# Performance work log

Measured on AMD Instinct MI355X. Metric: run time of the kernel, lower is better.

Reference implementation:

```python
import jax, jax.numpy as jnp
import numpy as np
from jax import lax

B, E, DIN = 16, 1024, 128   # batch, num_edges, link_state_dim
P, D = 2048, 128            # num_paths, path_state_dim


def _topology():
    # deterministic ragged paths: lengths in [4,16], at least one of max length 16
    lengths = 4 + (np.arange(P) % 13)
    idx = np.repeat(np.arange(P), lengths).astype(np.int32)          # path id per entry
    seqs = np.concatenate([np.arange(l) for l in lengths]).astype(np.int32)  # position in path
    paths = np.random.RandomState(0).randint(0, E, size=idx.shape[0]).astype(np.int32)
    return paths, idx, seqs


def setup_inputs() -> dict:
    key = jax.random.key(0)
    ks = jax.random.split(key, 8)
    paths, idx, seqs = _topology()
    s_in = 1.0 / np.sqrt(DIN)
    s_h = 1.0 / np.sqrt(D)
    return dict(
        inputs=jax.random.normal(ks[0], (B, E, DIN), jnp.float32),
        W_in=jax.random.normal(ks[1], (DIN, 3 * D), jnp.float32) * s_in,
        W_rec=jax.random.normal(ks[2], (D, 3 * D), jnp.float32) * s_h,
        b_in=jnp.zeros((3 * D,), jnp.float32),
        b_rec=jnp.zeros((3 * D,), jnp.float32),
        wq=jax.random.normal(ks[3], (D, D), jnp.float32) * s_h,
        wk=jax.random.normal(ks[4], (D, D), jnp.float32) * s_h,
        wv=jax.random.normal(ks[5], (D, D), jnp.float32) * s_h,
        paths=paths, idx=idx, seqs=seqs,
    )


def _forward(inputs, W_in, W_rec, b_in, b_rec, wq, wk, wv, paths, idx, seqs, max_len):
    Bc = inputs.shape[0]
    # --- ragged gather -> dense zero-padded tensor [B, P, max_len, DIN] (tf.gather + scatter_nd) ---
    h_tild = inputs[:, paths]                                  # [B, n_entries, DIN]
    link = jnp.zeros((Bc, P, max_len, DIN), inputs.dtype)
    link = link.at[:, idx, seqs].set(h_tild)
    x = link.reshape(Bc * P, max_len, DIN)                     # [BP, L, DIN]
    # --- GRU over time (keras GRUCell default: reset_after=True, tanh/sigmoid) ---
    xg = jnp.einsum('nld,de->lne', x, W_in) + b_in             # [L, BP, 3D]
    h0 = jnp.zeros((Bc * P, D), inputs.dtype)

    def step(h, xg_t):
        hg = h @ W_rec + b_rec                                 # [BP, 3D]
        xz, xr, xh = jnp.split(xg_t, 3, axis=-1)
        hz, hr, hh = jnp.split(hg, 3, axis=-1)
        z = jax.nn.sigmoid(xz + hz)
        r = jax.nn.sigmoid(xr + hr)
        hc = jnp.tanh(xh + r * hh)
        hn = z * h + (1.0 - z) * hc
        return hn, hn

    last, hs = lax.scan(step, h0, xg)                          # last:[BP,D], hs:[L,BP,D]
    hs = jnp.transpose(hs, (1, 0, 2))                          # [BP, L, D]
    # --- single-query QKV attention (raw scores, no softmax, as in source) ---
    key_ = hs @ wk                                             # [BP, L, D]
    val = hs @ wv                                              # [BP, L, D]
    q = last @ wq                                              # [BP, D]
    att = jnp.einsum('nld,nd->nl', key_, q)                    # [BP, L]
    ctx = jnp.einsum('nl,nld->nd', att, val)                   # [BP, D]
    return ctx.reshape(Bc, P, D)


def reference(inputs, W_in, W_rec, b_in, b_rec, wq, wk, wv, paths, idx, seqs):
    max_len = int(np.max(np.asarray(seqs))) + 1                # static (16)
    return _forward(inputs, W_in, W_rec, b_in, b_rec, wq, wk, wv, paths, idx, seqs, max_len)
```

## Files before the change

kernel.cpp:

```cpp
#include <hip/hip_runtime.h>
#include <hip/hip_bf16.h>
#include <cstddef>

#define P_ 2048
#define B_ 16
#define E_ 1024
#define D_ 128
#define L_ 16
#define TD_ 384

#define NEG_L2E (-1.44269504088896340736f)
#define TWO_L2E (2.88539008177792681472f)

typedef _Float16 f16x2 __attribute__((ext_vector_type(2)));
typedef _Float16 f16x8 __attribute__((ext_vector_type(8)));
typedef float    f32x4 __attribute__((ext_vector_type(4)));

__device__ __forceinline__ unsigned short f2h(float x) {
    _Float16 h = (_Float16)x;
    return __builtin_bit_cast(unsigned short, h);
}
__device__ __forceinline__ unsigned pk2(float a, float b) {
    return __builtin_bit_cast(unsigned, __builtin_amdgcn_cvt_pkrtz(a, b));
}
__device__ __forceinline__ float lo16(unsigned u) {
    return (float)__builtin_bit_cast(f16x2, u)[0];
}
__device__ __forceinline__ float hi16(unsigned u) {
    return (float)__builtin_bit_cast(f16x2, u)[1];
}
__device__ __forceinline__ float ex2(float x) {
#if __has_builtin(__builtin_amdgcn_exp2f)
    return __builtin_amdgcn_exp2f(x);
#else
    return exp2f(x);
#endif
}
__device__ __forceinline__ float dot2w(unsigned hu, unsigned qu, float c) {
#if __has_builtin(__builtin_amdgcn_fdot2)
    typedef __fp16 h2v __attribute__((ext_vector_type(2)));
    return __builtin_amdgcn_fdot2(__builtin_bit_cast(h2v, hu),
                                  __builtin_bit_cast(h2v, qu), c, false);
#else
    f16x2 h = __builtin_bit_cast(f16x2, hu), q = __builtin_bit_cast(f16x2, qu);
    return c + (float)h[0] * (float)q[0] + (float)h[1] * (float)q[1];
#endif
}

__device__ __forceinline__ void binv4(const float* __restrict__ d, float* __restrict__ o) {
    float f1 = d[0] * d[1];
    float f2 = f1 * d[2];
    float f3 = f2 * d[3];
    float r  = __builtin_amdgcn_rcpf(f3);
    o[3] = r * f2;
    float t  = r * d[3];
    o[2] = t * f1;
    float u  = t * d[2];
    o[1] = u * d[0];
    o[0] = u * d[1];
}

__device__ __forceinline__ void wf16(const float* __restrict__ src,
                                     unsigned short* __restrict__ dst, int g, int N,
                                     float sc) {
    int lane = g & 63, kt = (g >> 6) & 3, tile = g >> 8;
    int k0 = kt * 32 + (lane >> 4) * 8;
    int c = tile * 16 + (lane & 15);
#pragma unroll
    for (int j = 0; j < 8; ++j)
        dst[(size_t)g * 8 + j] = f2h(src[(size_t)(k0 + j) * N + c] * sc);
}

__device__ __forceinline__ void* hp(void* base, int t, int s, int boff) {
    return (char*)base + ((t * 16 + s) << 8) + (boff ^ ((s & 7) << 4));
}
__device__ __forceinline__ const void* hpc(const void* base, int t, int s, int boff) {
    return (const char*)base + ((t * 16 + s) << 8) + (boff ^ ((s & 7) << 4));
}

__global__ __launch_bounds__(256) void k_prep(const float* __restrict__ W_rec,
                                              const float* __restrict__ W_in,
                                              const float* __restrict__ wq,
                                              const float* __restrict__ wk,
                                              const float* __restrict__ wv,
                                              const int* __restrict__ paths,
                                              int* __restrict__ pt,
                                              unsigned short* __restrict__ WfR,
                                              unsigned short* __restrict__ WfI,
                                              unsigned short* __restrict__ wvf,
                                              float* __restrict__ M) {
    __shared__ float wk_lds[128 * 129];
    __shared__ float wq_row2[2][128];
    int blk = blockIdx.x, tid = threadIdx.x;
    if (blk < 128) {
        int gid = blk * 256 + tid;
        int p = gid >> 4, s = gid & 15;
        int c = p / 13, r = p - c * 13;
        int len = 4 + r;
        int off = 4 * p + 78 * c + (r * (r - 1)) / 2;
        pt[gid] = (s < len) ? paths[off + s] : E_;
        return;
    } else if (blk < 152) {
        int gg = (blk - 128) * 256 + tid;
        wf16(W_rec, WfR, gg, TD_, ((gg >> 8) < 16) ? NEG_L2E : TWO_L2E);
        return;
    } else if (blk < 176) {
        int gg = (blk - 152) * 256 + tid;
        wf16(W_in, WfI, gg, TD_, ((gg >> 8) < 16) ? NEG_L2E : TWO_L2E);
        return;
    } else if (blk < 184) {
        wf16(wv, wvf, (blk - 176) * 256 + tid, 128, 1.f);
        return;
    }
    int j0 = (blk - 184) * 2;
    int d = tid & 127, half = tid >> 7;
    for (int r = half * 64; r < half * 64 + 64; ++r)
        wk_lds[r * 129 + d] = wk[r * 128 + d];
    wq_row2[half][d] = wq[(j0 + half) * 128 + d];
    __syncthreads();
    float acc = 0.f;
    for (int k = 0; k < 128; ++k) acc += wq_row2[half][k] * wk_lds[d * 129 + k];
    M[(j0 + half) * 128 + d] = acc;
}

__global__ __launch_bounds__(256) void k_G(const float* __restrict__ inputs,
                                           const unsigned short* __restrict__ WfI,
                                           const float* __restrict__ b_in,
                                           const float* __restrict__ b_rec,
                                           unsigned short* __restrict__ G2,
                                           const float* __restrict__ M,
                                           unsigned short* __restrict__ Mf) {
    if (blockIdx.x >= 1024) {
        int tb = blockIdx.x - 1024;
        if (tb < 8) {
            wf16(M, Mf, tb * 256 + threadIdx.x, 128, 1.f);
        } else {
            for (int i = threadIdx.x; i < 2048; i += 256) {
                int bx = i >> 7, cc = i & 127;
                size_t base = ((size_t)(bx * (E_ + 1) + E_) * 128 + cc) * 4;
                G2[base]     = f2h((b_in[cc] + b_rec[cc]) * NEG_L2E);
                G2[base + 1] = f2h((b_in[128 + cc] + b_rec[128 + cc]) * NEG_L2E);
                G2[base + 2] = f2h(b_in[256 + cc] * TWO_L2E);
                G2[base + 3] = 0;
            }
        }
        return;
    }
    __shared__ __align__(16) unsigned short a_lds[16][136];
    __shared__ __align__(16) unsigned short g_lds[16][128][4];
    int tid = threadIdx.x, w = tid >> 6, L = tid & 63;
    int l15 = L & 15, q = L >> 4;
    int row0 = blockIdx.x * 16;
    int badd = row0 >> 10;
    {
        int r = tid >> 4, c = (tid & 15) * 8;
        const float4* p = (const float4*)(inputs + (size_t)(row0 + r) * 128 + c);
        float4 v0 = p[0], v1 = p[1];
        uint4 st;
        st.x = pk2(v0.x, v0.y); st.y = pk2(v0.z, v0.w);
        st.z = pk2(v1.x, v1.y); st.w = pk2(v1.z, v1.w);
        *(uint4*)&a_lds[r][c] = st;
    }
    __syncthreads();
    f16x8 af[4];
#pragma unroll
    for (int kt = 0; kt < 4; ++kt)
        af[kt] = *(const f16x8*)&a_lds[l15][kt * 32 + q * 8];
#pragma unroll
    for (int ct = 0; ct < 6; ++ct) {
        int tl = 6 * w + ct;
        f32x4 acc = (f32x4){0.f, 0.f, 0.f, 0.f};
#pragma unroll
        for (int kt = 0; kt < 4; ++kt)
            acc = __builtin_amdgcn_mfma_f32_16x16x32_f16(
                af[kt], *(const f16x8*)(WfI + (size_t)((tl * 4 + kt) * 64 + L) * 8), acc, 0, 0, 0);
        int g  = tl >> 3;
        int dd = (tl & 7) * 16 + l15;
        float sg  = (g < 2) ? NEG_L2E : TWO_L2E;
        float bia = (b_in[tl * 16 + l15] + (g < 2 ? b_rec[tl * 16 + l15] : 0.f)) * sg;
#pragma unroll
        for (int j = 0; j < 4; ++j) {
            int r = q * 4 + j;
            g_lds[r][dd][g] = f2h(acc[j] + bia);
        }
    }
    __syncthreads();
    {
        const uint4* src = (const uint4*)g_lds;
        uint4* dst = (uint4*)(G2 + (size_t)(row0 + badd) * 512);
#pragma unroll
        for (int i = 0; i < 4; ++i) dst[tid + 256 * i] = src[tid + 256 * i];
    }
}

__global__ __launch_bounds__(512, 4) void k_rec(const unsigned short* __restrict__ WfR,
                                                const float* __restrict__ b_rec,
                                                const unsigned short* __restrict__ G2,
                                                const int* __restrict__ pt,
                                                const unsigned short* __restrict__ Mf,
                                                const unsigned short* __restrict__ wvf,
                                                float* __restrict__ out) {
    __shared__ __align__(16) unsigned short hsl[16][16][128];
    __shared__ __align__(16) unsigned short qkb[16][136];
    __shared__ __align__(16) unsigned short svb[16][136];
    __shared__ float attp[2][16][16];
    __shared__ int ofs_lds[16][16];

    int tid = threadIdx.x, w = tid >> 6, L = tid & 63;
    int l15 = L & 15, q = L >> 4;
    int c0 = 16 * w + 4 * q;
    int n0 = blockIdx.x * 16;
    int b  = n0 >> 11;
    int p0 = n0 & (P_ - 1);
    int bb = b * (E_ + 1);

    f16x8 afw[3][4];
#pragma unroll
    for (int g = 0; g < 3; ++g)
#pragma unroll
        for (int kt = 0; kt < 4; ++kt)
            afw[g][kt] = *(const f16x8*)(WfR + (size_t)(((g * 8 + w) * 4 + kt) * 64 + L) * 8);

    if (tid < 256)
        ofs_lds[tid >> 4][tid & 15] = (bb + pt[p0 * L_ + tid]) << 10;

    f32x4 rh4;
#pragma unroll
    for (int j = 0; j < 4; ++j) rh4[j] = b_rec[256 + c0 + j] * TWO_L2E;
    float h_reg[4] = {0.f, 0.f, 0.f, 0.f};
    __syncthreads();

    int ofs[16];
    {
        const uint4* op = (const uint4*)&ofs_lds[l15][0];
        uint4 o0 = op[0], o1 = op[1], o2 = op[2], o3 = op[3];
        ofs[0]  = o0.x; ofs[1]  = o0.y; ofs[2]  = o0.z; ofs[3]  = o0.w;
        ofs[4]  = o1.x; ofs[5]  = o1.y; ofs[6]  = o1.z; ofs[7]  = o1.w;
        ofs[8]  = o2.x; ofs[9]  = o2.y; ofs[10] = o2.z; ofs[11] = o2.w;
        ofs[12] = o3.x; ofs[13] = o3.y; ofs[14] = o3.z; ofs[15] = o3.w;
    }

    const char* g2c = (const char*)G2 + (size_t)c0 * 8;
    uint4 cur0 = *(const uint4*)(g2c + ofs[0]);
    uint4 cur1 = *(const uint4*)(g2c + ofs[0] + 16);

#pragma unroll
    for (int t = 0; t < L_; ++t) {
        uint4 nx0 = cur0, nx1 = cur1;
        if (t < 15) {
            const char* gp = g2c + ofs[t + 1];
            nx0 = *(const uint4*)(gp);
            nx1 = *(const uint4*)(gp + 16);
        }

        float xh[4];
        f32x4 acc[3];
        acc[0][0] = lo16(cur0.x); acc[0][1] = lo16(cur0.z);
        acc[0][2] = lo16(cur1.x); acc[0][3] = lo16(cur1.z);
        acc[1][0] = hi16(cur0.x); acc[1][1] = hi16(cur0.z);
        acc[1][2] = hi16(cur1.x); acc[1][3] = hi16(cur1.z);
        xh[0] = lo16(cur0.y); xh[1] = lo16(cur0.w);
        xh[2] = lo16(cur1.y); xh[3] = lo16(cur1.w);
        acc[2] = rh4;

        if (t > 0) {
            f16x8 hf[4];
#pragma unroll
            for (int kt = 0; kt < 4; ++kt)
                hf[kt] = *(const f16x8*)hpc(hsl, t - 1, l15, kt * 64 + q * 16);
#pragma unroll
            for (int g = 0; g < 3; ++g)
#pragma unroll
                for (int kt = 0; kt < 4; ++kt)
                    acc[g] = __builtin_amdgcn_mfma_f32_16x16x32_f16(afw[g][kt], hf[kt], acc[g], 0, 0, 0);
        }

        float dz[4], dr[4];
#pragma unroll
        for (int j = 0; j < 4; ++j) {
            dz[j] = 1.f + ex2(acc[0][j]);
            dr[j] = 1.f + ex2(acc[1][j]);
        }
        float z4[4], r4[4];
        binv4(dz, z4);
        binv4(dr, r4);
        float dh[4];
#pragma unroll
        for (int j = 0; j < 4; ++j)
            dh[j] = 1.f + ex2(fminf(xh[j] + r4[j] * acc[2][j], 30.f));
        float y4[4];
        binv4(dh, y4);
        float hn[4];
#pragma unroll
        for (int j = 0; j < 4; ++j) {
            float hc = 1.f - 2.f * y4[j];
            hn[j] = hc + z4[j] * (h_reg[j] - hc);
            h_reg[j] = hn[j];
        }
        uint2 st;
        st.x = pk2(hn[0], hn[1]); st.y = pk2(hn[2], hn[3]);
        *(uint2*)hp(hsl, t, l15, c0 * 2) = st;
        cur0 = nx0; cur1 = nx1;

        __builtin_amdgcn_wave_barrier();
        __builtin_amdgcn_s_waitcnt(0xC07F);
        __builtin_amdgcn_s_barrier();
        __builtin_amdgcn_wave_barrier();
    }

    {
        f16x8 hf[4];
#pragma unroll
        for (int kt = 0; kt < 4; ++kt)
            hf[kt] = *(const f16x8*)hpc(hsl, 15, l15, kt * 64 + q * 16);
        f32x4 a = (f32x4){0.f, 0.f, 0.f, 0.f};
#pragma unroll
        for (int kt = 0; kt < 4; ++kt)
            a = __builtin_amdgcn_mfma_f32_16x16x32_f16(
                *(const f16x8*)(Mf + (size_t)((w * 4 + kt) * 64 + L) * 8), hf[kt], a, 0, 0, 0);
        uint2 st;
        st.x = pk2(a[0], a[1]); st.y = pk2(a[2], a[3]);
        *(uint2*)&qkb[l15][c0] = st;
    }
    __syncthreads();

    {
        int s = tid & 15, l = (tid >> 4) & 15, half = tid >> 8;
        const uint4* qr = (const uint4*)&qkb[s][half * 64];
        float a = 0.f;
#pragma unroll
        for (int k8 = 0; k8 < 8; ++k8) {
            uint4 hh = *(const uint4*)hpc(hsl, l, s, half * 128 + k8 * 16);
            uint4 qq = qr[k8];
            a = dot2w(hh.x, qq.x, a); a = dot2w(hh.y, qq.y, a);
            a = dot2w(hh.z, qq.z, a); a = dot2w(hh.w, qq.w, a);
        }
        attp[half][s][l] = a;
    }
    __syncthreads();

    {
        int s = tid >> 5, d0 = (tid & 31) * 4;
        float v[4] = {0.f, 0.f, 0.f, 0.f};
#pragma unroll
        for (int l = 0; l < 16; ++l) {
            float a = attp[0][s][l] + attp[1][s][l];
            uint2 hu = *(const uint2*)hpc(hsl, l, s, d0 * 2);
            v[0] += a * lo16(hu.x); v[1] += a * hi16(hu.x);
            v[2] += a * lo16(hu.y); v[3] += a * hi16(hu.y);
        }
        uint2 st;
        st.x = pk2(v[0], v[1]); st.y = pk2(v[2], v[3]);
        *(uint2*)&svb[s][d0] = st;
    }
    __syncthreads();

    {
        f16x8 sf[4];
#pragma unroll
        for (int kt = 0; kt < 4; ++kt)
            sf[kt] = *(const f16x8*)&svb[l15][kt * 32 + q * 8];
        f32x4 a = (f32x4){0.f, 0.f, 0.f, 0.f};
#pragma unroll
        for (int kt = 0; kt < 4; ++kt)
            a = __builtin_amdgcn_mfma_f32_16x16x32_f16(
                *(const f16x8*)(wvf + (size_t)((w * 4 + kt) * 64 + L) * 8), sf[kt], a, 0, 0, 0);
        *(f32x4*)&out[(size_t)(n0 + l15) * D_ + c0] = a;
    }
}

extern "C" void kernel_launch(void* const* d_in, const int* in_sizes, int n_in,
                              void* d_out, int out_size, void* d_ws, size_t ws_size,
                              hipStream_t stream) {
    const float* inputs = (const float*)d_in[0];
    const float* W_in   = (const float*)d_in[1];
    const float* W_rec  = (const float*)d_in[2];
    const float* b_in   = (const float*)d_in[3];
    const float* b_rec  = (const float*)d_in[4];
    const float* wq     = (const float*)d_in[5];
    const float* wk     = (const float*)d_in[6];
    const float* wvp    = (const float*)d_in[7];
    const int* paths    = (const int*)d_in[8];

    const size_t off_pt  = 0;
    const size_t off_WfR = off_pt  + (size_t)P_ * L_ * 4;
    const size_t off_WfI = off_WfR + (size_t)24 * 256 * 16;
    const size_t off_Mf  = off_WfI + (size_t)24 * 256 * 16;
    const size_t off_wvf = off_Mf  + (size_t)8 * 256 * 16;
    const size_t off_M   = off_wvf + (size_t)8 * 256 * 16;
    const size_t off_G2  = off_M   + (size_t)128 * 128 * 4;
    char* ws = (char*)d_ws;
    int* pt             = (int*)(ws + off_pt);
    unsigned short* WfR = (unsigned short*)(ws + off_WfR);
    unsigned short* WfI = (unsigned short*)(ws + off_WfI);
    unsigned short* Mf  = (unsigned short*)(ws + off_Mf);
    unsigned short* wvf = (unsigned short*)(ws + off_wvf);
    float* M            = (float*)(ws + off_M);
    unsigned short* G2  = (unsigned short*)(ws + off_G2);
    float* out = (float*)d_out;

    k_prep<<<dim3(248), dim3(256), 0, stream>>>(W_rec, W_in, wq, wk, wvp, paths,
                                                pt, WfR, WfI, wvf, M);
    k_G<<<dim3(1024 + 8 + 1), dim3(256), 0, stream>>>(inputs, WfI, b_in, b_rec,
                                                      G2, M, Mf);
    k_rec<<<dim3(B_ * P_ / 16), dim3(512), 0, stream>>>(WfR, b_rec, G2, pt,
                                                        Mf, wvf, out);
}
```

Measured before the change: 173.6 us.

## Rebalance prep work across kernels, cut k_rec registers, drop batched reciprocals

Moves the path-table, W_rec and wv conversions out of k_prep into extra blocks of k_G, and has k_prep write M straight into the fp16 MFMA layout, so the separate fp32 M buffer and its conversion pass go away. In k_rec, the 16 per-lane gather offsets are now read from LDS each step instead of being held in registers. The batched reciprocal trick (binv4) is replaced by one rcp per gate element. The launch-bounds hint for k_rec drops from 4 to 2 waves per SIMD, which lets the compiler use more registers, possibly at the cost of occupancy.

```diff
diff --git a/kernel.cpp b/kernel.cpp
--- a/kernel.cpp
+++ b/kernel.cpp
@@ -47,19 +47,6 @@
 #endif
 }
 
-__device__ __forceinline__ void binv4(const float* __restrict__ d, float* __restrict__ o) {
-    float f1 = d[0] * d[1];
-    float f2 = f1 * d[2];
-    float f3 = f2 * d[3];
-    float r  = __builtin_amdgcn_rcpf(f3);
-    o[3] = r * f2;
-    float t  = r * d[3];
-    o[2] = t * f1;
-    float u  = t * d[2];
-    o[1] = u * d[0];
-    o[0] = u * d[1];
-}
-
 __device__ __forceinline__ void wf16(const float* __restrict__ src,
                                      unsigned short* __restrict__ dst, int g, int N,
                                      float sc) {
@@ -78,41 +65,20 @@
     return (const char*)base + ((t * 16 + s) << 8) + (boff ^ ((s & 7) << 4));
 }
 
-__global__ __launch_bounds__(256) void k_prep(const float* __restrict__ W_rec,
-                                              const float* __restrict__ W_in,
+__global__ __launch_bounds__(256) void k_prep(const float* __restrict__ W_in,
                                               const float* __restrict__ wq,
                                               const float* __restrict__ wk,
-                                              const float* __restrict__ wv,
-                                              const int* __restrict__ paths,
-                                              int* __restrict__ pt,
-                                              unsigned short* __restrict__ WfR,
                                               unsigned short* __restrict__ WfI,
-                                              unsigned short* __restrict__ wvf,
-                                              float* __restrict__ M) {
+                                              unsigned short* __restrict__ Mf) {
     __shared__ float wk_lds[128 * 129];
     __shared__ float wq_row2[2][128];
     int blk = blockIdx.x, tid = threadIdx.x;
-    if (blk < 128) {
-        int gid = blk * 256 + tid;
-        int p = gid >> 4, s = gid & 15;
-        int c = p / 13, r = p - c * 13;
-        int len = 4 + r;
-        int off = 4 * p + 78 * c + (r * (r - 1)) / 2;
-        pt[gid] = (s < len) ? paths[off + s] : E_;
-        return;
-    } else if (blk < 152) {
-        int gg = (blk - 128) * 256 + tid;
-        wf16(W_rec, WfR, gg, TD_, ((gg >> 8) < 16) ? NEG_L2E : TWO_L2E);
-        return;
-    } else if (blk < 176) {
-        int gg = (blk - 152) * 256 + tid;
+    if (blk < 24) {
+        int gg = blk * 256 + tid;
         wf16(W_in, WfI, gg, TD_, ((gg >> 8) < 16) ? NEG_L2E : TWO_L2E);
         return;
-    } else if (blk < 184) {
-        wf16(wv, wvf, (blk - 176) * 256 + tid, 128, 1.f);
-        return;
-    }
-    int j0 = (blk - 184) * 2;
+    }
+    int j0 = (blk - 24) * 2;
     int d = tid & 127, half = tid >> 7;
     for (int r = half * 64; r < half * 64 + 64; ++r)
         wk_lds[r * 129 + d] = wk[r * 128 + d];
@@ -120,7 +86,12 @@
     __syncthreads();
     float acc = 0.f;
     for (int k = 0; k < 128; ++k) acc += wq_row2[half][k] * wk_lds[d * 129 + k];
-    M[(j0 + half) * 128 + d] = acc;
+    {
+        int r = j0 + half;
+        int tile = d >> 4, kt = r >> 5;
+        int ln = ((r >> 3) & 3) * 16 + (d & 15), jj = r & 7;
+        Mf[((size_t)(tile * 4 + kt) * 64 + ln) * 8 + jj] = f2h(acc);
+    }
 }
 
 __global__ __launch_bounds__(256) void k_G(const float* __restrict__ inputs,
@@ -128,14 +99,28 @@
                                            const float* __restrict__ b_in,
                                            const float* __restrict__ b_rec,
                                            unsigned short* __restrict__ G2,
-                                           const float* __restrict__ M,
-                                           unsigned short* __restrict__ Mf) {
+                                           const float* __restrict__ W_rec,
+                                           const float* __restrict__ wv,
+                                           const int* __restrict__ paths,
+                                           int* __restrict__ pt,
+                                           unsigned short* __restrict__ WfR,
+                                           unsigned short* __restrict__ wvf) {
     if (blockIdx.x >= 1024) {
-        int tb = blockIdx.x - 1024;
-        if (tb < 8) {
-            wf16(M, Mf, tb * 256 + threadIdx.x, 128, 1.f);
+        int tb = blockIdx.x - 1024, tid = threadIdx.x;
+        if (tb < 128) {
+            int gid = tb * 256 + tid;
+            int p = gid >> 4, s = gid & 15;
+            int c = p / 13, r = p - c * 13;
+            int len = 4 + r;
+            int off = 4 * p + 78 * c + (r * (r - 1)) / 2;
+            pt[gid] = (s < len) ? paths[off + s] : E_;
+        } else if (tb < 152) {
+            int gg = (tb - 128) * 256 + tid;
+            wf16(W_rec, WfR, gg, TD_, ((gg >> 8) < 16) ? NEG_L2E : TWO_L2E);
+        } else if (tb < 160) {
+            wf16(wv, wvf, (tb - 152) * 256 + tid, 128, 1.f);
         } else {
-            for (int i = threadIdx.x; i < 2048; i += 256) {
+            for (int i = tid; i < 2048; i += 256) {
                 int bx = i >> 7, cc = i & 127;
                 size_t base = ((size_t)(bx * (E_ + 1) + E_) * 128 + cc) * 4;
                 G2[base]     = f2h((b_in[cc] + b_rec[cc]) * NEG_L2E);
@@ -193,7 +178,7 @@
     }
 }
 
-__global__ __launch_bounds__(512, 4) void k_rec(const unsigned short* __restrict__ WfR,
+__global__ __launch_bounds__(512, 2) void k_rec(const unsigned short* __restrict__ WfR,
                                                 const float* __restrict__ b_rec,
                                                 const unsigned short* __restrict__ G2,
                                                 const int* __restrict__ pt,
@@ -230,25 +215,18 @@
     float h_reg[4] = {0.f, 0.f, 0.f, 0.f};
     __syncthreads();
 
-    int ofs[16];
-    {
-        const uint4* op = (const uint4*)&ofs_lds[l15][0];
-        uint4 o0 = op[0], o1 = op[1], o2 = op[2], o3 = op[3];
-        ofs[0]  = o0.x; ofs[1]  = o0.y; ofs[2]  = o0.z; ofs[3]  = o0.w;
-        ofs[4]  = o1.x; ofs[5]  = o1.y; ofs[6]  = o1.z; ofs[7]  = o1.w;
-        ofs[8]  = o2.x; ofs[9]  = o2.y; ofs[10] = o2.z; ofs[11] = o2.w;
-        ofs[12] = o3.x; ofs[13] = o3.y; ofs[14] = o3.z; ofs[15] = o3.w;
-    }
-
     const char* g2c = (const char*)G2 + (size_t)c0 * 8;
-    uint4 cur0 = *(const uint4*)(g2c + ofs[0]);
-    uint4 cur1 = *(const uint4*)(g2c + ofs[0] + 16);
+    int ocur = ofs_lds[l15][0];
+    uint4 cur0 = *(const uint4*)(g2c + ocur);
+    uint4 cur1 = *(const uint4*)(g2c + ocur + 16);
 
 #pragma unroll
     for (int t = 0; t < L_; ++t) {
         uint4 nx0 = cur0, nx1 = cur1;
+        int onext = ocur;
         if (t < 15) {
-            const char* gp = g2c + ofs[t + 1];
+            onext = ofs_lds[l15][t + 1];
+            const char* gp = g2c + onext;
             nx0 = *(const uint4*)(gp);
             nx1 = *(const uint4*)(gp + 16);
         }
@@ -275,32 +253,24 @@
                     acc[g] = __builtin_amdgcn_mfma_f32_16x16x32_f16(afw[g][kt], hf[kt], acc[g], 0, 0, 0);
         }
 
-        float dz[4], dr[4];
+        float z4[4], r4[4];
 #pragma unroll
         for (int j = 0; j < 4; ++j) {
-            dz[j] = 1.f + ex2(acc[0][j]);
-            dr[j] = 1.f + ex2(acc[1][j]);
-        }
-        float z4[4], r4[4];
-        binv4(dz, z4);
-        binv4(dr, r4);
-        float dh[4];
-#pragma unroll
-        for (int j = 0; j < 4; ++j)
-            dh[j] = 1.f + ex2(fminf(xh[j] + r4[j] * acc[2][j], 30.f));
-        float y4[4];
-        binv4(dh, y4);
+            z4[j] = __builtin_amdgcn_rcpf(1.f + ex2(acc[0][j]));
+            r4[j] = __builtin_amdgcn_rcpf(1.f + ex2(acc[1][j]));
+        }
         float hn[4];
 #pragma unroll
         for (int j = 0; j < 4; ++j) {
-            float hc = 1.f - 2.f * y4[j];
+            float pre = fminf(xh[j] + r4[j] * acc[2][j], 30.f);
+            float hc  = 1.f - 2.f * __builtin_amdgcn_rcpf(1.f + ex2(pre));
             hn[j] = hc + z4[j] * (h_reg[j] - hc);
             h_reg[j] = hn[j];
         }
         uint2 st;
         st.x = pk2(hn[0], hn[1]); st.y = pk2(hn[2], hn[3]);
         *(uint2*)hp(hsl, t, l15, c0 * 2) = st;
-        cur0 = nx0; cur1 = nx1;
+        cur0 = nx0; cur1 = nx1; ocur = onext;
 
         __builtin_amdgcn_wave_barrier();
         __builtin_amdgcn_s_waitcnt(0xC07F);
@@ -387,22 +357,19 @@
     const size_t off_WfI = off_WfR + (size_t)24 * 256 * 16;
     const size_t off_Mf  = off_WfI + (size_t)24 * 256 * 16;
     const size_t off_wvf = off_Mf  + (size_t)8 * 256 * 16;
-    const size_t off_M   = off_wvf + (size_t)8 * 256 * 16;
-    const size_t off_G2  = off_M   + (size_t)128 * 128 * 4;
+    const size_t off_G2  = off_wvf + (size_t)8 * 256 * 16;
     char* ws = (char*)d_ws;
     int* pt             = (int*)(ws + off_pt);
     unsigned short* WfR = (unsigned short*)(ws + off_WfR);
     unsigned short* WfI = (unsigned short*)(ws + off_WfI);
     unsigned short* Mf  = (unsigned short*)(ws + off_Mf);
     unsigned short* wvf = (unsigned short*)(ws + off_wvf);
-    float* M            = (float*)(ws + off_M);
     unsigned short* G2  = (unsigned short*)(ws + off_G2);
     float* out = (float*)d_out;
 
-    k_prep<<<dim3(248), dim3(256), 0, stream>>>(W_rec, W_in, wq, wk, wvp, paths,
-                                                pt, WfR, WfI, wvf, M);
-    k_G<<<dim3(1024 + 8 + 1), dim3(256), 0, stream>>>(inputs, WfI, b_in, b_rec,
-                                                      G2, M, Mf);
+    k_prep<<<dim3(88), dim3(256), 0, stream>>>(W_in, wq, wk, WfI, Mf);
+    k_G<<<dim3(1024 + 161), dim3(256), 0, stream>>>(inputs, WfI, b_in, b_rec, G2,
+                                                    W_rec, wvp, paths, pt, WfR, wvf);
     k_rec<<<dim3(B_ * P_ / 16), dim3(512), 0, stream>>>(WfR, b_rec, G2, pt,
                                                         Mf, wvf, out);
 }
```

After: 175.3 us. About the same (+1.0%).
